# Optimization experiments

Measured on AMD Instinct MI355X. Metric: run time of the kernel, lower is better.

The kernel has to match this reference:

```python
import jax, jax.numpy as jnp
import numpy as np

N = 200000
B = 2
GX, GY, GZ = 480, 360, 32          # full-res voxel grid for input_coords
GX2, GY2, GZ2 = 240, 180, 16       # output_scale grid for bxyz_indx
CIN, CR, COUT = 64, 64, 64
CR2 = CR // 2
P_SCALE = (2, 4, 6, 8)


def setup_inputs() -> dict:
    key = jax.random.key(0)
    ks = jax.random.split(key, 24)
    s = 0.05
    input_data = jax.random.normal(ks[0], (N, CIN), dtype=jnp.float32)
    bcol = jax.random.randint(ks[1], (N, 1), 0, B, dtype=jnp.int32)
    xc = jax.random.randint(ks[2], (N, 1), 0, GX, dtype=jnp.int32)
    yc = jax.random.randint(ks[3], (N, 1), 0, GY, dtype=jnp.int32)
    zc = jax.random.randint(ks[4], (N, 1), 0, GZ, dtype=jnp.int32)
    input_coords = jnp.concatenate([bcol, xc, yc, zc], axis=1)
    input_coords_inv = jax.random.randint(ks[5], (N,), 0, N, dtype=jnp.int32)
    b2 = jax.random.randint(ks[6], (N, 1), 0, B, dtype=jnp.int32)
    x2 = jax.random.randint(ks[7], (N, 1), 0, GX2, dtype=jnp.int32)
    y2 = jax.random.randint(ks[8], (N, 1), 0, GY2, dtype=jnp.int32)
    z2 = jax.random.randint(ks[9], (N, 1), 0, GZ2, dtype=jnp.int32)
    bxyz_indx = jnp.concatenate([b2, x2, y2, z2], axis=1)
    # parameters (torch Linear stored here as [in, out])
    W_red = jax.random.normal(ks[10], (CIN, CR)) * s
    b_red = jnp.zeros((CR,), jnp.float32)
    fc_list_W = jax.random.normal(ks[11], (4, CR, CR2)) * s
    fc_list_b = jnp.zeros((4, CR2), jnp.float32)
    fcs_W = jax.random.normal(ks[12], (4, CR2, CR2)) * s
    fcs_b = jnp.zeros((4, CR2), jnp.float32)
    fc_W = jax.random.normal(ks[13], (CR2, CR2)) * s
    out_fc_W = jax.random.normal(ks[14], (CR2, CR)) * s
    lo_W1 = jax.random.normal(ks[15], (2 * CR, CR)) * s
    lo_W2 = jax.random.normal(ks[16], (CR, COUT)) * s
    lo_b2 = jnp.zeros((COUT,), jnp.float32)
    return dict(input_data=input_data, input_coords=input_coords,
                input_coords_inv=input_coords_inv, bxyz_indx=bxyz_indx,
                W_red=W_red, b_red=b_red, fc_list_W=fc_list_W, fc_list_b=fc_list_b,
                fcs_W=fcs_W, fcs_b=fcs_b, fc_W=fc_W, out_fc_W=out_fc_W,
                lo_W1=lo_W1, lo_W2=lo_W2, lo_b2=lo_b2)


def _segment_mean(x, seg, num_segments):
    sums = jax.ops.segment_sum(x, seg, num_segments=num_segments)
    cnt = jax.ops.segment_sum(jnp.ones((x.shape[0], 1), x.dtype), seg,
                              num_segments=num_segments)
    return sums / jnp.maximum(cnt, 1.0)


def reference(input_data, input_coords, input_coords_inv, bxyz_indx,
              W_red, b_red, fc_list_W, fc_list_b, fcs_W, fcs_b,
              fc_W, out_fc_W, lo_W1, lo_W2, lo_b2):
    reduced = jax.nn.relu(input_data @ W_red + b_red)          # [N, CR]
    bcol = input_coords[:, 0]
    xyz = input_coords[:, 1:]
    outs = []
    for j, ps in enumerate(P_SCALE):
        dx = (GX - 1) // ps + 1
        dy = (GY - 1) // ps + 1
        dz = (GZ - 1) // ps + 1
        q = xyz // ps                                          # [N, 3]
        # dense linearized voxel id replaces torch.unique(return_inverse)
        lin = ((bcol * dx + q[:, 0]) * dy + q[:, 1]) * dz + q[:, 2]
        nseg = B * dx * dy * dz
        fkm = _segment_mean(reduced, lin, nseg)                # [nseg, CR]
        att = jax.nn.relu(fkm @ fc_list_W[j] + fc_list_b[j])   # [nseg, CR2]
        outs.append(att[lin])                                  # gather back [N, CR2]
    scale_features = jnp.stack(outs, axis=1)                   # [N, 4, CR2]
    feat_S = scale_features.sum(axis=1)                        # [N, CR2]
    feat_Z = jax.nn.relu(feat_S @ fc_W)                        # [N, CR2]
    att_v = jax.nn.sigmoid(jnp.einsum('nc,kcd->nkd', feat_Z, fcs_W) + fcs_b)
    fused = (scale_features * att_v).sum(axis=1) @ out_fc_W    # [N, CR]
    output_f = jnp.concatenate([reduced, fused], axis=1)       # [N, 2*CR]
    proj = jax.nn.relu(output_f @ lo_W1) @ lo_W2 + lo_b2       # [N, COUT]
    proj = proj[input_coords_inv]
    # with_fm branch: index = (b, z, y, x) of bxyz_indx (b,x,y,z)
    lin2 = ((bxyz_indx[:, 0] * GZ2 + bxyz_indx[:, 3]) * GY2
            + bxyz_indx[:, 2]) * GX2 + bxyz_indx[:, 1]
    tv_fmap = jax.ops.segment_max(proj, lin2, num_segments=B * GZ2 * GY2 * GX2)
    tv_fmap = jnp.where(jnp.isneginf(tv_fmap), 0.0, tv_fmap)   # empty voxels -> 0
    return proj, tv_fmap, lin2
```

## Files before the change

### kernel.cpp

```cpp
#include <hip/hip_runtime.h>
#include <math.h>

#define NPTS   200000
#define CR     64
#define CR2    32

#define NSEG0      1382400
#define SUM123_ROW2 172800
#define SUM123_ROW3 230400
#define SUM123_ROWS 252000

#define TVSEG  1382400
#define GX2    240
#define GY2    180
#define GZ2    16

#define NBATCH 21600

__device__ __forceinline__ float bcastf(float v, int l) {
    return __int_as_float(__builtin_amdgcn_readlane(__float_as_int(v), l));
}

__device__ __forceinline__ int lin_scale(int b, int x, int y, int z,
                                         int ps, int dx, int dy, int dz) {
    int qx = x / ps, qy = y / ps, qz = z / ps;
    return ((b * dx + qx) * dy + qy) * dz + qz;
}

__device__ __forceinline__ void seg_decode(int seg, int& l1, int& l2, int& l3) {
    int qz = seg & 15; int rest = seg >> 4;
    int qy = rest % 180; int rest2 = rest / 180;
    int qx = rest2 % 240; int bb = rest2 / 240;
    l1 = ((bb * 120 + (qx >> 1)) * 90 + (qy >> 1)) * 8 + (qz >> 1);
    l2 = ((bb *  80 + (qx / 3)) * 60 + (qy / 3)) * 6 + (qz / 3);
    l3 = ((bb *  60 + (qx >> 2)) * 45 + (qy >> 2)) * 4 + (qz >> 2);
}

__global__ __launch_bounds__(256) void k_reduced(
        const float* __restrict__ in, const float* __restrict__ Wred,
        const float* __restrict__ bred, float* __restrict__ red) {
    __shared__ float Wl[CR * CR];
    for (int i = threadIdx.x; i < CR * CR; i += blockDim.x) Wl[i] = Wred[i];
    __syncthreads();
    int lane = threadIdx.x & 63;
    float bl = bred[lane];
    int wid  = blockIdx.x * 4 + (threadIdx.x >> 6);
    int nw   = gridDim.x * 4;
    for (int p = wid; p < NPTS / 2; p += nw) {
        int r0 = 2 * p, r1 = r0 + 1;
        float x0 = in[(size_t)r0 * CR + lane];
        float x1 = in[(size_t)r1 * CR + lane];
        float acc0 = bl, acc1 = bl;
#pragma unroll
        for (int k = 0; k < CR; ++k) {
            float w = Wl[k * CR + lane];
            acc0 += bcastf(x0, k) * w;
            acc1 += bcastf(x1, k) * w;
        }
        red[(size_t)r0 * CR + lane] = fmaxf(acc0, 0.f);
        red[(size_t)r1 * CR + lane] = fmaxf(acc1, 0.f);
    }
}

__global__ __launch_bounds__(256) void k_scatter(
        const float* __restrict__ red, const int* __restrict__ coords,
        float* __restrict__ sum0, float* __restrict__ cnt) {
    int lane = threadIdx.x & 63;
    int wid  = blockIdx.x * 4 + (threadIdx.x >> 6);
    int nw   = gridDim.x * 4;
    for (int r = wid; r < NPTS; r += nw) {
        int4 c = ((const int4*)coords)[r];
        int l0 = lin_scale(c.x, c.y, c.z, c.w, 2, 240, 180, 16);
        float v = red[(size_t)r * CR + lane];
        atomicAdd(&sum0[(size_t)l0 * CR + lane], v);
        if (lane == 0) atomicAdd(&cnt[l0], 1.0f);
    }
}

__global__ __launch_bounds__(256) void k_gatt(
        const float* __restrict__ sum0, float* __restrict__ attbuf,
        const float* __restrict__ cnt,
        const float* __restrict__ fcW, const float* __restrict__ fcB) {
    __shared__ float sw[3 * CR * CR2];
    for (int i = threadIdx.x; i < 3 * CR * CR2; i += blockDim.x)
        sw[i] = fcW[CR * CR2 + i];
    __syncthreads();
    int lane = threadIdx.x & 63;
    int d = lane & 31;
    int wid = blockIdx.x * 4 + (threadIdx.x >> 6);
    int nw  = gridDim.x * 4;
    for (int s = wid; s < SUM123_ROWS; s += nw) {
        int childLin = -1;
        const float* w; float bj;
        if (s < SUM123_ROW2) {
            int qz = s & 7, t = s >> 3;
            int qy = t % 90, t2 = t / 90;
            int qx = t2 % 120, b = t2 / 120;
            if (lane < 8) {
                int i = (lane >> 2) & 1, j = (lane >> 1) & 1, k = lane & 1;
                childLin = ((b * 240 + 2 * qx + i) * 180 + 2 * qy + j) * 16 + 2 * qz + k;
            }
            w = sw; bj = fcB[1 * CR2 + d];
        } else if (s < SUM123_ROW3) {
            int s2 = s - SUM123_ROW2;
            int qz = s2 % 6, t = s2 / 6;
            int qy = t % 60, t2 = t / 60;
            int qx = t2 % 80, b = t2 / 80;
            if (lane < 27) {
                int i = lane / 9, j = (lane / 3) % 3, k = lane % 3;
                int cz = 3 * qz + k;
                if (cz < 16)
                    childLin = ((b * 240 + 3 * qx + i) * 180 + 3 * qy + j) * 16 + cz;
            }
            w = sw + 2048; bj = fcB[2 * CR2 + d];
        } else {
            int s3 = s - SUM123_ROW3;
            int qz = s3 & 3, t = s3 >> 2;
            int qy = t % 45, t2 = t / 45;
            int qx = t2 % 60, b = t2 / 60;
            int i = lane >> 4, j = (lane >> 2) & 3, k = lane & 3;
            childLin = ((b * 240 + 4 * qx + i) * 180 + 4 * qy + j) * 16 + 4 * qz + k;
            w = sw + 4096; bj = fcB[3 * CR2 + d];
        }
        float myc = (childLin >= 0) ? cnt[childLin] : 0.f;
        unsigned long long mask = __ballot(myc > 0.f);
        if (!mask) continue;
        float ctot = myc;
        ctot += __shfl_xor(ctot, 1, 64);
        ctot += __shfl_xor(ctot, 2, 64);
        ctot += __shfl_xor(ctot, 4, 64);
        ctot += __shfl_xor(ctot, 8, 64);
        ctot += __shfl_xor(ctot, 16, 64);
        ctot += __shfl_xor(ctot, 32, 64);
        float acc = 0.f;
        while (mask) {
            int j = __ffsll((long long)mask) - 1; mask &= mask - 1;
            int cl = __builtin_amdgcn_readlane(childLin, j);
            acc += sum0[(size_t)cl * CR + lane];
        }
        float m = acc * (1.f / ctot);
        float p = bj;
#pragma unroll
        for (int k = 0; k < CR; ++k)
            p += bcastf(m, k) * w[k * CR2 + d];
        float att = fmaxf(p, 0.f);
        if (lane < 32) attbuf[(size_t)s * CR2 + lane] = att;
    }
}

__global__ __launch_bounds__(256) void k_att0(
        float* __restrict__ tv, const float* __restrict__ cnt,
        const float* __restrict__ fcW, const float* __restrict__ fcB) {
    __shared__ float sw[CR * CR2];
    for (int i = threadIdx.x; i < CR * CR2; i += blockDim.x) sw[i] = fcW[i];
    __syncthreads();
    int lane = threadIdx.x & 63;
    int d = lane & 31;
    int h = lane >> 5;
    float b0 = fcB[d];
    int wid = blockIdx.x * 4 + (threadIdx.x >> 6);
    int nw  = gridDim.x * 4;
    for (int batch = wid; batch < NBATCH; batch += nw) {
        int base = batch * 64;
        float c = cnt[base + lane];
        unsigned long long mask = __ballot(c > 0.f);
        while (mask) {
            int j0 = __ffsll((long long)mask) - 1; mask &= mask - 1;
            int j1 = j0, j2 = j0, j3 = j0;
            if (mask) { j1 = __ffsll((long long)mask) - 1; mask &= mask - 1;
              if (mask) { j2 = __ffsll((long long)mask) - 1; mask &= mask - 1;
                if (mask) { j3 = __ffsll((long long)mask) - 1; mask &= mask - 1; } } }
            float* row0 = tv + (size_t)(base + j0) * CR;
            float* row1 = tv + (size_t)(base + j1) * CR;
            float* row2 = tv + (size_t)(base + j2) * CR;
            float* row3 = tv + (size_t)(base + j3) * CR;
            float m0 = row0[lane] * (1.f / bcastf(c, j0));
            float m1 = row1[lane] * (1.f / bcastf(c, j1));
            float m2 = row2[lane] * (1.f / bcastf(c, j2));
            float m3 = row3[lane] * (1.f / bcastf(c, j3));
            float p0 = b0, p1 = b0, p2 = b0, p3 = b0;
#pragma unroll
            for (int k = 0; k < CR; ++k) {
                float wk = sw[k * CR2 + d];
                p0 += bcastf(m0, k) * wk;
                p1 += bcastf(m1, k) * wk;
                p2 += bcastf(m2, k) * wk;
                p3 += bcastf(m3, k) * wk;
            }
            float a0 = fmaxf(p0, 0.f), a1 = fmaxf(p1, 0.f);
            float a2 = fmaxf(p2, 0.f), a3 = fmaxf(p3, 0.f);
            float* rA = h ? row1 : row0; float vA = h ? a1 : a0;
            float* rB = h ? row3 : row2; float vB = h ? a3 : a2;
            rA[d] = vA;
            rB[d] = vB;
        }
    }
}

__global__ __launch_bounds__(1024) void k_mm(
        const float* __restrict__ outW, const float* __restrict__ loW1,
        float* __restrict__ M) {
    int e = threadIdx.x + blockIdx.x * 1024;
    if (e >= 2048) return;
    int r = e >> 6, c = e & 63;
    float acc = 0.f;
#pragma unroll
    for (int k = 0; k < 64; ++k)
        acc += outW[r * 64 + k] * loW1[(64 + k) * 64 + c];
    M[e] = acc;
}

__global__ __launch_bounds__(256) void k_seg(
        float* __restrict__ tv, const float* __restrict__ attbuf,
        const float* __restrict__ cnt,
        const float* __restrict__ fc_W, const float* __restrict__ fcsW,
        const float* __restrict__ fcsB, const float* __restrict__ M) {
    __shared__ float s_fcZ[1024];
    __shared__ float s_fcs[4096];
    __shared__ float s_M[2048];
    for (int i = threadIdx.x; i < 1024; i += 256) s_fcZ[i]  = fc_W[i];
    for (int i = threadIdx.x; i < 4096; i += 256) s_fcs[i]  = fcsW[i];
    for (int i = threadIdx.x; i < 2048; i += 256) s_M[i]    = M[i];
    __syncthreads();

    int lane = threadIdx.x & 63;
    int d = lane & 31;
    int h = lane >> 5;
    float vbA = fcsB[(h ? 1 : 0) * CR2 + d];
    float vbB = fcsB[(h ? 3 : 2) * CR2 + d];
    const float* VA = s_fcs + (h ? 1 : 0) * 1024;
    const float* VB = s_fcs + (h ? 3 : 2) * 1024;

    int wid = blockIdx.x * 4 + (threadIdx.x >> 6);
    int nw  = gridDim.x * 4;
    for (int batch = wid; batch < NBATCH; batch += nw) {
        int base = batch * 64;
        float c = cnt[base + lane];
        unsigned long long mask = __ballot(c > 0.f);
        while (mask) {
            int j0 = __ffsll((long long)mask) - 1; mask &= mask - 1;
            int n = 1, j1 = j0, j2 = j0, j3 = j0;
            if (mask) { j1 = __ffsll((long long)mask) - 1; mask &= mask - 1; n = 2;
              if (mask) { j2 = __ffsll((long long)mask) - 1; mask &= mask - 1; n = 3;
                if (mask) { j3 = __ffsll((long long)mask) - 1; mask &= mask - 1; n = 4; } } }
            int seg0 = base + j0, seg1 = base + j1, seg2 = base + j2, seg3 = base + j3;
            float* row0 = tv + (size_t)seg0 * CR;
            float* row1 = tv + (size_t)seg1 * CR;
            float* row2 = tv + (size_t)seg2 * CR;
            float* row3 = tv + (size_t)seg3 * CR;

            int l1_0, l2_0, l3_0, l1_1, l2_1, l3_1;
            int l1_2, l2_2, l3_2, l1_3, l2_3, l3_3;
            seg_decode(seg0, l1_0, l2_0, l3_0);
            seg_decode(seg1, l1_1, l2_1, l3_1);
            seg_decode(seg2, l1_2, l2_2, l3_2);
            seg_decode(seg3, l1_3, l2_3, l3_3);

            float a0_0 = row0[d];
            float a0_1 = row1[d];
            float a0_2 = row2[d];
            float a0_3 = row3[d];
            float a1_0 = attbuf[(size_t)l1_0 * CR2 + d];
            float a2_0 = attbuf[(size_t)(SUM123_ROW2 + l2_0) * CR2 + d];
            float a3_0 = attbuf[(size_t)(SUM123_ROW3 + l3_0) * CR2 + d];
            float a1_1 = attbuf[(size_t)l1_1 * CR2 + d];
            float a2_1 = attbuf[(size_t)(SUM123_ROW2 + l2_1) * CR2 + d];
            float a3_1 = attbuf[(size_t)(SUM123_ROW3 + l3_1) * CR2 + d];
            float a1_2 = attbuf[(size_t)l1_2 * CR2 + d];
            float a2_2 = attbuf[(size_t)(SUM123_ROW2 + l2_2) * CR2 + d];
            float a3_2 = attbuf[(size_t)(SUM123_ROW3 + l3_2) * CR2 + d];
            float a1_3 = attbuf[(size_t)l1_3 * CR2 + d];
            float a2_3 = attbuf[(size_t)(SUM123_ROW2 + l2_3) * CR2 + d];
            float a3_3 = attbuf[(size_t)(SUM123_ROW3 + l3_3) * CR2 + d];

            float fS0 = a0_0 + a1_0 + a2_0 + a3_0;
            float fS1 = a0_1 + a1_1 + a2_1 + a3_1;
            float fS2 = a0_2 + a1_2 + a2_2 + a3_2;
            float fS3 = a0_3 + a1_3 + a2_3 + a3_3;

            float z0 = 0.f, z1 = 0.f, z2 = 0.f, z3 = 0.f;
#pragma unroll
            for (int cc = 0; cc < CR2; ++cc) {
                float wz = s_fcZ[cc * CR2 + d];
                z0 += bcastf(fS0, cc) * wz;
                z1 += bcastf(fS1, cc) * wz;
                z2 += bcastf(fS2, cc) * wz;
                z3 += bcastf(fS3, cc) * wz;
            }
            float fZ0 = fmaxf(z0, 0.f), fZ1 = fmaxf(z1, 0.f);
            float fZ2 = fmaxf(z2, 0.f), fZ3 = fmaxf(z3, 0.f);

            float avA0 = vbA, avA1 = vbA, avA2 = vbA, avA3 = vbA;
            float avB0 = vbB, avB1 = vbB, avB2 = vbB, avB3 = vbB;
#pragma unroll
            for (int cc = 0; cc < CR2; ++cc) {
                float wa = VA[cc * CR2 + d];
                float wb = VB[cc * CR2 + d];
                float f0 = bcastf(fZ0, cc), f1 = bcastf(fZ1, cc);
                float f2 = bcastf(fZ2, cc), f3 = bcastf(fZ3, cc);
                avA0 += f0 * wa; avB0 += f0 * wb;
                avA1 += f1 * wa; avB1 += f1 * wb;
                avA2 += f2 * wa; avB2 += f2 * wb;
                avA3 += f3 * wa; avB3 += f3 * wb;
            }
            avA0 = 1.f / (1.f + __expf(-avA0)); avB0 = 1.f / (1.f + __expf(-avB0));
            avA1 = 1.f / (1.f + __expf(-avA1)); avB1 = 1.f / (1.f + __expf(-avB1));
            avA2 = 1.f / (1.f + __expf(-avA2)); avB2 = 1.f / (1.f + __expf(-avB2));
            avA3 = 1.f / (1.f + __expf(-avA3)); avB3 = 1.f / (1.f + __expf(-avB3));

            float u0 = (h ? a1_0 : a0_0) * avA0 + (h ? a3_0 : a2_0) * avB0;
            float u1 = (h ? a1_1 : a0_1) * avA1 + (h ? a3_1 : a2_1) * avB1;
            float u2 = (h ? a1_2 : a0_2) * avA2 + (h ? a3_2 : a2_2) * avB2;
            float u3 = (h ? a1_3 : a0_3) * avA3 + (h ? a3_3 : a2_3) * avB3;
            float fI0 = u0 + __shfl_xor(u0, 32, 64);
            float fI1 = u1 + __shfl_xor(u1, 32, 64);
            float fI2 = u2 + __shfl_xor(u2, 32, 64);
            float fI3 = u3 + __shfl_xor(u3, 32, 64);

            float g0 = 0.f, g1 = 0.f, g2 = 0.f, g3 = 0.f;
#pragma unroll
            for (int dd = 0; dd < CR2; ++dd) {
                float wm = s_M[dd * CR + lane];
                g0 += bcastf(fI0, dd) * wm;
                g1 += bcastf(fI1, dd) * wm;
                g2 += bcastf(fI2, dd) * wm;
                g3 += bcastf(fI3, dd) * wm;
            }
            row0[lane] = g0;
            if (n > 1) row1[lane] = g1;
            if (n > 2) row2[lane] = g2;
            if (n > 3) row3[lane] = g3;
        }
    }
}

__global__ __launch_bounds__(256) void k_pg(
        const float* __restrict__ red, const float* __restrict__ gtab,
        const int* __restrict__ coords, const int* __restrict__ inv,
        const float* __restrict__ loW1, const float* __restrict__ loW2,
        const float* __restrict__ lob2, float* __restrict__ outProj) {
    __shared__ float s_W1[4096];
    __shared__ float s_W2[4096];
    for (int i = threadIdx.x; i < 4096; i += 256) s_W1[i] = loW1[i];
    for (int i = threadIdx.x; i < 4096; i += 256) s_W2[i] = loW2[i];
    __syncthreads();

    int lane = threadIdx.x & 63;
    float lob = lob2[lane];
    int wid = blockIdx.x * 4 + (threadIdx.x >> 6);
    int nw  = gridDim.x * 4;
    for (int q = wid; q < NPTS / 4; q += nw) {
        int i0 = 4 * q, i1 = i0 + 1, i2 = i0 + 2, i3 = i0 + 3;
        int s0 = inv[i0], s1 = inv[i1], s2 = inv[i2], s3 = inv[i3];
        int4 c0 = ((const int4*)coords)[s0];
        int4 c1 = ((const int4*)coords)[s1];
        int4 c2 = ((const int4*)coords)[s2];
        int4 c3 = ((const int4*)coords)[s3];
        int l0 = lin_scale(c0.x, c0.y, c0.z, c0.w, 2, 240, 180, 16);
        int l1 = lin_scale(c1.x, c1.y, c1.z, c1.w, 2, 240, 180, 16);
        int l2 = lin_scale(c2.x, c2.y, c2.z, c2.w, 2, 240, 180, 16);
        int l3 = lin_scale(c3.x, c3.y, c3.z, c3.w, 2, 240, 180, 16);

        float x0 = red[(size_t)s0 * CR + lane];
        float x1 = red[(size_t)s1 * CR + lane];
        float x2 = red[(size_t)s2 * CR + lane];
        float x3 = red[(size_t)s3 * CR + lane];
        float h0 = gtab[(size_t)l0 * CR + lane];
        float h1 = gtab[(size_t)l1 * CR + lane];
        float h2 = gtab[(size_t)l2 * CR + lane];
        float h3 = gtab[(size_t)l3 * CR + lane];
#pragma unroll
        for (int k = 0; k < CR; ++k) {
            float w = s_W1[k * CR + lane];
            h0 += bcastf(x0, k) * w;
            h1 += bcastf(x1, k) * w;
            h2 += bcastf(x2, k) * w;
            h3 += bcastf(x3, k) * w;
        }
        h0 = fmaxf(h0, 0.f); h1 = fmaxf(h1, 0.f);
        h2 = fmaxf(h2, 0.f); h3 = fmaxf(h3, 0.f);

        float q0 = lob, q1 = lob, q2 = lob, q3 = lob;
#pragma unroll
        for (int k = 0; k < CR; ++k) {
            float w = s_W2[k * CR + lane];
            q0 += bcastf(h0, k) * w;
            q1 += bcastf(h1, k) * w;
            q2 += bcastf(h2, k) * w;
            q3 += bcastf(h3, k) * w;
        }
        outProj[(size_t)i0 * CR + lane] = q0;
        outProj[(size_t)i1 * CR + lane] = q1;
        outProj[(size_t)i2 * CR + lane] = q2;
        outProj[(size_t)i3 * CR + lane] = q3;
    }
}

__global__ __launch_bounds__(256) void k_clear(
        float* __restrict__ tv, const float* __restrict__ cnt) {
    int lane = threadIdx.x & 63;
    int wid = blockIdx.x * 4 + (threadIdx.x >> 6);
    int nw = gridDim.x * 4;
    for (int batch = wid; batch < NBATCH; batch += nw) {
        int base = batch * 64;
        float c = cnt[base + lane];
        unsigned long long mask = __ballot(c > 0.f);
        while (mask) {
            int j = __ffsll((long long)mask) - 1; mask &= mask - 1;
            tv[(size_t)(base + j) * CR + lane] = 0.f;
        }
    }
}

__device__ __forceinline__ unsigned int fkey(float f) {
    unsigned int b = __float_as_uint(f);
    return (b & 0x80000000u) ? ~b : (b | 0x80000000u);
}

__global__ __launch_bounds__(256) void k_scatmax(
        const float* __restrict__ outProj, const int* __restrict__ bxyz,
        float* __restrict__ outLin, unsigned int* __restrict__ tvKey,
        unsigned char* __restrict__ flags) {
    int lane = threadIdx.x & 63;
    int wid  = blockIdx.x * 4 + (threadIdx.x >> 6);
    int nw   = gridDim.x * 4;
    for (int i = wid; i < NPTS; i += nw) {
        float v = outProj[(size_t)i * CR + lane];
        int4 c = ((const int4*)bxyz)[i];
        int lin2 = ((c.x * GZ2 + c.w) * GY2 + c.z) * GX2 + c.y;
        if (lane == 0) {
            outLin[i] = (float)lin2;
            flags[lin2] = 1;
        }
        atomicMax(&tvKey[(size_t)lin2 * CR + lane], fkey(v));
    }
}

__global__ __launch_bounds__(256) void k_fix(
        unsigned int* __restrict__ tv, const unsigned char* __restrict__ flags) {
    int lane = threadIdx.x & 63;
    int wid = blockIdx.x * 4 + (threadIdx.x >> 6);
    int nw  = gridDim.x * 4;
    for (int batch = wid; batch < NBATCH; batch += nw) {
        int base = batch * 64;
        unsigned char f = flags[base + lane];
        unsigned long long mask = __ballot(f != 0);
        while (mask) {
            int j = __ffsll((long long)mask) - 1; mask &= mask - 1;
            size_t idx = (size_t)(base + j) * CR + lane;
            unsigned int k = tv[idx];
            float v = (k == 0u) ? 0.f
                    : __uint_as_float((k & 0x80000000u) ? (k & 0x7FFFFFFFu) : ~k);
            ((float*)tv)[idx] = v;
        }
    }
}

extern "C" void kernel_launch(void* const* d_in, const int* in_sizes, int n_in,
                              void* d_out, int out_size, void* d_ws, size_t ws_size,
                              hipStream_t stream) {
    (void)in_sizes; (void)n_in; (void)out_size; (void)ws_size;
    const float* in_data = (const float*)d_in[0];
    const int*   coords  = (const int*)d_in[1];
    const int*   inv     = (const int*)d_in[2];
    const int*   bxyz    = (const int*)d_in[3];
    const float* W_red   = (const float*)d_in[4];
    const float* b_red   = (const float*)d_in[5];
    const float* fcW     = (const float*)d_in[6];
    const float* fcB     = (const float*)d_in[7];
    const float* fcsW    = (const float*)d_in[8];
    const float* fcsB    = (const float*)d_in[9];
    const float* fc_W    = (const float*)d_in[10];
    const float* outW    = (const float*)d_in[11];
    const float* loW1    = (const float*)d_in[12];
    const float* loW2    = (const float*)d_in[13];
    const float* lob2    = (const float*)d_in[14];

    float* outProj = (float*)d_out;
    float* tv      = outProj + (size_t)NPTS * CR;
    float* outLin  = tv + (size_t)TVSEG * CR;

    float* ws_f   = (float*)d_ws;
    float* red    = ws_f;
    float* attbuf = red + (size_t)NPTS * CR;
    float* cnt    = attbuf + (size_t)SUM123_ROWS * CR2;
    float* Mmat   = cnt + (size_t)NSEG0;
    unsigned char* flags = (unsigned char*)(Mmat + 2048);

    hipMemsetAsync(tv, 0, (size_t)TVSEG * CR * sizeof(float), stream);
    hipMemsetAsync(cnt, 0, (size_t)NSEG0 * sizeof(float), stream);
    hipMemsetAsync(flags, 0, (size_t)TVSEG, stream);

    k_mm<<<2, 1024, 0, stream>>>(outW, loW1, Mmat);
    k_reduced<<<1024, 256, 0, stream>>>(in_data, W_red, b_red, red);
    k_scatter<<<4096, 256, 0, stream>>>(red, coords, tv, cnt);
    k_gatt<<<2048, 256, 0, stream>>>(tv, attbuf, cnt, fcW, fcB);
    k_att0<<<2048, 256, 0, stream>>>(tv, cnt, fcW, fcB);
    k_seg<<<2048, 256, 0, stream>>>(tv, attbuf, cnt, fc_W, fcsW, fcsB, Mmat);
    k_pg<<<1024, 256, 0, stream>>>(red, tv, coords, inv, loW1, loW2, lob2, outProj);
    k_clear<<<512, 256, 0, stream>>>(tv, cnt);
    k_scatmax<<<1024, 256, 0, stream>>>(outProj, bxyz, outLin, (unsigned int*)tv, flags);
    k_fix<<<512, 256, 0, stream>>>((unsigned int*)tv, flags);
}
```

Baseline: 1.192 ms.

## Build compact occupied-segment list and fuse reduce/scatter and projection/scatter-max kernels

Fuses the reduction GEMM with the scale-0 scatter, and during that scatter builds a compact list of occupied segments plus a rank table. The att0 and seg kernels then iterate over that list instead of ballot-scanning all 1.38M segments, and write into compact buffers. att0 also clears the tv rows, which removes the separate clear kernel. The projection and scatter-max kernels are merged, so outProj is no longer re-read. In exchange the scatter gains a global atomic counter, list order becomes nondeterministic, and the gather in the projection kernel goes through an extra rank indirection.

```diff
diff --git a/kernel.cpp b/kernel.cpp
--- a/kernel.cpp
+++ b/kernel.cpp
@@ -36,9 +36,12 @@
     l3 = ((bb *  60 + (qx >> 2)) * 45 + (qy >> 2)) * 4 + (qz >> 2);
 }
 
-__global__ __launch_bounds__(256) void k_reduced(
-        const float* __restrict__ in, const float* __restrict__ Wred,
-        const float* __restrict__ bred, float* __restrict__ red) {
+__global__ __launch_bounds__(256) void k_redscat(
+        const float* __restrict__ in, const int* __restrict__ coords,
+        const float* __restrict__ Wred, const float* __restrict__ bred,
+        float* __restrict__ red, float* __restrict__ sum0,
+        float* __restrict__ cnt, int* __restrict__ list0,
+        int* __restrict__ listCount, int* __restrict__ rankArr) {
     __shared__ float Wl[CR * CR];
     for (int i = threadIdx.x; i < CR * CR; i += blockDim.x) Wl[i] = Wred[i];
     __syncthreads();
@@ -57,23 +60,27 @@
             acc0 += bcastf(x0, k) * w;
             acc1 += bcastf(x1, k) * w;
         }
-        red[(size_t)r0 * CR + lane] = fmaxf(acc0, 0.f);
-        red[(size_t)r1 * CR + lane] = fmaxf(acc1, 0.f);
-    }
-}
-
-__global__ __launch_bounds__(256) void k_scatter(
-        const float* __restrict__ red, const int* __restrict__ coords,
-        float* __restrict__ sum0, float* __restrict__ cnt) {
-    int lane = threadIdx.x & 63;
-    int wid  = blockIdx.x * 4 + (threadIdx.x >> 6);
-    int nw   = gridDim.x * 4;
-    for (int r = wid; r < NPTS; r += nw) {
-        int4 c = ((const int4*)coords)[r];
-        int l0 = lin_scale(c.x, c.y, c.z, c.w, 2, 240, 180, 16);
-        float v = red[(size_t)r * CR + lane];
-        atomicAdd(&sum0[(size_t)l0 * CR + lane], v);
-        if (lane == 0) atomicAdd(&cnt[l0], 1.0f);
+        acc0 = fmaxf(acc0, 0.f); acc1 = fmaxf(acc1, 0.f);
+        red[(size_t)r0 * CR + lane] = acc0;
+        red[(size_t)r1 * CR + lane] = acc1;
+        int4 c0 = ((const int4*)coords)[r0];
+        int4 c1 = ((const int4*)coords)[r1];
+        int l0a = lin_scale(c0.x, c0.y, c0.z, c0.w, 2, 240, 180, 16);
+        int l0b = lin_scale(c1.x, c1.y, c1.z, c1.w, 2, 240, 180, 16);
+        atomicAdd(&sum0[(size_t)l0a * CR + lane], acc0);
+        atomicAdd(&sum0[(size_t)l0b * CR + lane], acc1);
+        if (lane == 0) {
+            float olda = atomicAdd(&cnt[l0a], 1.0f);
+            if (olda == 0.f) {
+                int idx = atomicAdd(listCount, 1);
+                list0[idx] = l0a; rankArr[l0a] = idx;
+            }
+            float oldb = atomicAdd(&cnt[l0b], 1.0f);
+            if (oldb == 0.f) {
+                int idx = atomicAdd(listCount, 1);
+                list0[idx] = l0b; rankArr[l0b] = idx;
+            }
+        }
     }
 }
 
@@ -148,9 +155,11 @@
     }
 }
 
-__global__ __launch_bounds__(256) void k_att0(
+__global__ __launch_bounds__(256) void k_att0z(
         float* __restrict__ tv, const float* __restrict__ cnt,
-        const float* __restrict__ fcW, const float* __restrict__ fcB) {
+        const int* __restrict__ list0, const int* __restrict__ listCount,
+        const float* __restrict__ fcW, const float* __restrict__ fcB,
+        float* __restrict__ att0c) {
     __shared__ float sw[CR * CR2];
     for (int i = threadIdx.x; i < CR * CR2; i += blockDim.x) sw[i] = fcW[i];
     __syncthreads();
@@ -158,42 +167,38 @@
     int d = lane & 31;
     int h = lane >> 5;
     float b0 = fcB[d];
+    int total = listCount[0];
+    int ngroups = (total + 3) >> 2;
     int wid = blockIdx.x * 4 + (threadIdx.x >> 6);
     int nw  = gridDim.x * 4;
-    for (int batch = wid; batch < NBATCH; batch += nw) {
-        int base = batch * 64;
-        float c = cnt[base + lane];
-        unsigned long long mask = __ballot(c > 0.f);
-        while (mask) {
-            int j0 = __ffsll((long long)mask) - 1; mask &= mask - 1;
-            int j1 = j0, j2 = j0, j3 = j0;
-            if (mask) { j1 = __ffsll((long long)mask) - 1; mask &= mask - 1;
-              if (mask) { j2 = __ffsll((long long)mask) - 1; mask &= mask - 1;
-                if (mask) { j3 = __ffsll((long long)mask) - 1; mask &= mask - 1; } } }
-            float* row0 = tv + (size_t)(base + j0) * CR;
-            float* row1 = tv + (size_t)(base + j1) * CR;
-            float* row2 = tv + (size_t)(base + j2) * CR;
-            float* row3 = tv + (size_t)(base + j3) * CR;
-            float m0 = row0[lane] * (1.f / bcastf(c, j0));
-            float m1 = row1[lane] * (1.f / bcastf(c, j1));
-            float m2 = row2[lane] * (1.f / bcastf(c, j2));
-            float m3 = row3[lane] * (1.f / bcastf(c, j3));
-            float p0 = b0, p1 = b0, p2 = b0, p3 = b0;
-#pragma unroll
-            for (int k = 0; k < CR; ++k) {
-                float wk = sw[k * CR2 + d];
-                p0 += bcastf(m0, k) * wk;
-                p1 += bcastf(m1, k) * wk;
-                p2 += bcastf(m2, k) * wk;
-                p3 += bcastf(m3, k) * wk;
-            }
-            float a0 = fmaxf(p0, 0.f), a1 = fmaxf(p1, 0.f);
-            float a2 = fmaxf(p2, 0.f), a3 = fmaxf(p3, 0.f);
-            float* rA = h ? row1 : row0; float vA = h ? a1 : a0;
-            float* rB = h ? row3 : row2; float vB = h ? a3 : a2;
-            rA[d] = vA;
-            rB[d] = vB;
-        }
+    for (int g = wid; g < ngroups; g += nw) {
+        int r0 = 4 * g;
+        int r1 = min(r0 + 1, total - 1);
+        int r2 = min(r0 + 2, total - 1);
+        int r3 = min(r0 + 3, total - 1);
+        int s0 = list0[r0], s1 = list0[r1], s2 = list0[r2], s3 = list0[r3];
+        float* row0 = tv + (size_t)s0 * CR;
+        float* row1 = tv + (size_t)s1 * CR;
+        float* row2 = tv + (size_t)s2 * CR;
+        float* row3 = tv + (size_t)s3 * CR;
+        float m0 = row0[lane] * (1.f / cnt[s0]);
+        float m1 = row1[lane] * (1.f / cnt[s1]);
+        float m2 = row2[lane] * (1.f / cnt[s2]);
+        float m3 = row3[lane] * (1.f / cnt[s3]);
+        float p0 = b0, p1 = b0, p2 = b0, p3 = b0;
+#pragma unroll
+        for (int k = 0; k < CR; ++k) {
+            float wk = sw[k * CR2 + d];
+            p0 += bcastf(m0, k) * wk;
+            p1 += bcastf(m1, k) * wk;
+            p2 += bcastf(m2, k) * wk;
+            p3 += bcastf(m3, k) * wk;
+        }
+        float a0 = fmaxf(p0, 0.f), a1 = fmaxf(p1, 0.f);
+        float a2 = fmaxf(p2, 0.f), a3 = fmaxf(p3, 0.f);
+        att0c[(size_t)(h ? r2 : r0) * CR2 + d] = h ? a2 : a0;
+        att0c[(size_t)(h ? r3 : r1) * CR2 + d] = h ? a3 : a1;
+        row0[lane] = 0.f; row1[lane] = 0.f; row2[lane] = 0.f; row3[lane] = 0.f;
     }
 }
 
@@ -211,10 +216,11 @@
 }
 
 __global__ __launch_bounds__(256) void k_seg(
-        float* __restrict__ tv, const float* __restrict__ attbuf,
-        const float* __restrict__ cnt,
+        const int* __restrict__ list0, const int* __restrict__ listCount,
+        const float* __restrict__ att0c, const float* __restrict__ attbuf,
         const float* __restrict__ fc_W, const float* __restrict__ fcsW,
-        const float* __restrict__ fcsB, const float* __restrict__ M) {
+        const float* __restrict__ fcsB, const float* __restrict__ M,
+        float* __restrict__ gc) {
     __shared__ float s_fcZ[1024];
     __shared__ float s_fcs[4096];
     __shared__ float s_M[2048];
@@ -231,114 +237,115 @@
     const float* VA = s_fcs + (h ? 1 : 0) * 1024;
     const float* VB = s_fcs + (h ? 3 : 2) * 1024;
 
+    int total = listCount[0];
+    int ngroups = (total + 3) >> 2;
     int wid = blockIdx.x * 4 + (threadIdx.x >> 6);
     int nw  = gridDim.x * 4;
-    for (int batch = wid; batch < NBATCH; batch += nw) {
-        int base = batch * 64;
-        float c = cnt[base + lane];
-        unsigned long long mask = __ballot(c > 0.f);
-        while (mask) {
-            int j0 = __ffsll((long long)mask) - 1; mask &= mask - 1;
-            int n = 1, j1 = j0, j2 = j0, j3 = j0;
-            if (mask) { j1 = __ffsll((long long)mask) - 1; mask &= mask - 1; n = 2;
-              if (mask) { j2 = __ffsll((long long)mask) - 1; mask &= mask - 1; n = 3;
-                if (mask) { j3 = __ffsll((long long)mask) - 1; mask &= mask - 1; n = 4; } } }
-            int seg0 = base + j0, seg1 = base + j1, seg2 = base + j2, seg3 = base + j3;
-            float* row0 = tv + (size_t)seg0 * CR;
-            float* row1 = tv + (size_t)seg1 * CR;
-            float* row2 = tv + (size_t)seg2 * CR;
-            float* row3 = tv + (size_t)seg3 * CR;
-
-            int l1_0, l2_0, l3_0, l1_1, l2_1, l3_1;
-            int l1_2, l2_2, l3_2, l1_3, l2_3, l3_3;
-            seg_decode(seg0, l1_0, l2_0, l3_0);
-            seg_decode(seg1, l1_1, l2_1, l3_1);
-            seg_decode(seg2, l1_2, l2_2, l3_2);
-            seg_decode(seg3, l1_3, l2_3, l3_3);
-
-            float a0_0 = row0[d];
-            float a0_1 = row1[d];
-            float a0_2 = row2[d];
-            float a0_3 = row3[d];
-            float a1_0 = attbuf[(size_t)l1_0 * CR2 + d];
-            float a2_0 = attbuf[(size_t)(SUM123_ROW2 + l2_0) * CR2 + d];
-            float a3_0 = attbuf[(size_t)(SUM123_ROW3 + l3_0) * CR2 + d];
-            float a1_1 = attbuf[(size_t)l1_1 * CR2 + d];
-            float a2_1 = attbuf[(size_t)(SUM123_ROW2 + l2_1) * CR2 + d];
-            float a3_1 = attbuf[(size_t)(SUM123_ROW3 + l3_1) * CR2 + d];
-            float a1_2 = attbuf[(size_t)l1_2 * CR2 + d];
-            float a2_2 = attbuf[(size_t)(SUM123_ROW2 + l2_2) * CR2 + d];
-            float a3_2 = attbuf[(size_t)(SUM123_ROW3 + l3_2) * CR2 + d];
-            float a1_3 = attbuf[(size_t)l1_3 * CR2 + d];
-            float a2_3 = attbuf[(size_t)(SUM123_ROW2 + l2_3) * CR2 + d];
-            float a3_3 = attbuf[(size_t)(SUM123_ROW3 + l3_3) * CR2 + d];
-
-            float fS0 = a0_0 + a1_0 + a2_0 + a3_0;
-            float fS1 = a0_1 + a1_1 + a2_1 + a3_1;
-            float fS2 = a0_2 + a1_2 + a2_2 + a3_2;
-            float fS3 = a0_3 + a1_3 + a2_3 + a3_3;
-
-            float z0 = 0.f, z1 = 0.f, z2 = 0.f, z3 = 0.f;
-#pragma unroll
-            for (int cc = 0; cc < CR2; ++cc) {
-                float wz = s_fcZ[cc * CR2 + d];
-                z0 += bcastf(fS0, cc) * wz;
-                z1 += bcastf(fS1, cc) * wz;
-                z2 += bcastf(fS2, cc) * wz;
-                z3 += bcastf(fS3, cc) * wz;
-            }
-            float fZ0 = fmaxf(z0, 0.f), fZ1 = fmaxf(z1, 0.f);
-            float fZ2 = fmaxf(z2, 0.f), fZ3 = fmaxf(z3, 0.f);
-
-            float avA0 = vbA, avA1 = vbA, avA2 = vbA, avA3 = vbA;
-            float avB0 = vbB, avB1 = vbB, avB2 = vbB, avB3 = vbB;
-#pragma unroll
-            for (int cc = 0; cc < CR2; ++cc) {
-                float wa = VA[cc * CR2 + d];
-                float wb = VB[cc * CR2 + d];
-                float f0 = bcastf(fZ0, cc), f1 = bcastf(fZ1, cc);
-                float f2 = bcastf(fZ2, cc), f3 = bcastf(fZ3, cc);
-                avA0 += f0 * wa; avB0 += f0 * wb;
-                avA1 += f1 * wa; avB1 += f1 * wb;
-                avA2 += f2 * wa; avB2 += f2 * wb;
-                avA3 += f3 * wa; avB3 += f3 * wb;
-            }
-            avA0 = 1.f / (1.f + __expf(-avA0)); avB0 = 1.f / (1.f + __expf(-avB0));
-            avA1 = 1.f / (1.f + __expf(-avA1)); avB1 = 1.f / (1.f + __expf(-avB1));
-            avA2 = 1.f / (1.f + __expf(-avA2)); avB2 = 1.f / (1.f + __expf(-avB2));
-            avA3 = 1.f / (1.f + __expf(-avA3)); avB3 = 1.f / (1.f + __expf(-avB3));
-
-            float u0 = (h ? a1_0 : a0_0) * avA0 + (h ? a3_0 : a2_0) * avB0;
-            float u1 = (h ? a1_1 : a0_1) * avA1 + (h ? a3_1 : a2_1) * avB1;
-            float u2 = (h ? a1_2 : a0_2) * avA2 + (h ? a3_2 : a2_2) * avB2;
-            float u3 = (h ? a1_3 : a0_3) * avA3 + (h ? a3_3 : a2_3) * avB3;
-            float fI0 = u0 + __shfl_xor(u0, 32, 64);
-            float fI1 = u1 + __shfl_xor(u1, 32, 64);
-            float fI2 = u2 + __shfl_xor(u2, 32, 64);
-            float fI3 = u3 + __shfl_xor(u3, 32, 64);
-
-            float g0 = 0.f, g1 = 0.f, g2 = 0.f, g3 = 0.f;
-#pragma unroll
-            for (int dd = 0; dd < CR2; ++dd) {
-                float wm = s_M[dd * CR + lane];
-                g0 += bcastf(fI0, dd) * wm;
-                g1 += bcastf(fI1, dd) * wm;
-                g2 += bcastf(fI2, dd) * wm;
-                g3 += bcastf(fI3, dd) * wm;
-            }
-            row0[lane] = g0;
-            if (n > 1) row1[lane] = g1;
-            if (n > 2) row2[lane] = g2;
-            if (n > 3) row3[lane] = g3;
-        }
-    }
-}
-
-__global__ __launch_bounds__(256) void k_pg(
-        const float* __restrict__ red, const float* __restrict__ gtab,
+    for (int g = wid; g < ngroups; g += nw) {
+        int r0 = 4 * g;
+        int r1 = min(r0 + 1, total - 1);
+        int r2 = min(r0 + 2, total - 1);
+        int r3 = min(r0 + 3, total - 1);
+        int seg0 = list0[r0], seg1 = list0[r1], seg2 = list0[r2], seg3 = list0[r3];
+
+        int l1_0, l2_0, l3_0, l1_1, l2_1, l3_1;
+        int l1_2, l2_2, l3_2, l1_3, l2_3, l3_3;
+        seg_decode(seg0, l1_0, l2_0, l3_0);
+        seg_decode(seg1, l1_1, l2_1, l3_1);
+        seg_decode(seg2, l1_2, l2_2, l3_2);
+        seg_decode(seg3, l1_3, l2_3, l3_3);
+
+        float a0_0 = att0c[(size_t)r0 * CR2 + d];
+        float a0_1 = att0c[(size_t)r1 * CR2 + d];
+        float a0_2 = att0c[(size_t)r2 * CR2 + d];
+        float a0_3 = att0c[(size_t)r3 * CR2 + d];
+        float a1_0 = attbuf[(size_t)l1_0 * CR2 + d];
+        float a2_0 = attbuf[(size_t)(SUM123_ROW2 + l2_0) * CR2 + d];
+        float a3_0 = attbuf[(size_t)(SUM123_ROW3 + l3_0) * CR2 + d];
+        float a1_1 = attbuf[(size_t)l1_1 * CR2 + d];
+        float a2_1 = attbuf[(size_t)(SUM123_ROW2 + l2_1) * CR2 + d];
+        float a3_1 = attbuf[(size_t)(SUM123_ROW3 + l3_1) * CR2 + d];
+        float a1_2 = attbuf[(size_t)l1_2 * CR2 + d];
+        float a2_2 = attbuf[(size_t)(SUM123_ROW2 + l2_2) * CR2 + d];
+        float a3_2 = attbuf[(size_t)(SUM123_ROW3 + l3_2) * CR2 + d];
+        float a1_3 = attbuf[(size_t)l1_3 * CR2 + d];
+        float a2_3 = attbuf[(size_t)(SUM123_ROW2 + l2_3) * CR2 + d];
+        float a3_3 = attbuf[(size_t)(SUM123_ROW3 + l3_3) * CR2 + d];
+
+        float fS0 = a0_0 + a1_0 + a2_0 + a3_0;
+        float fS1 = a0_1 + a1_1 + a2_1 + a3_1;
+        float fS2 = a0_2 + a1_2 + a2_2 + a3_2;
+        float fS3 = a0_3 + a1_3 + a2_3 + a3_3;
+
+        float z0 = 0.f, z1 = 0.f, z2 = 0.f, z3 = 0.f;
+#pragma unroll
+        for (int cc = 0; cc < CR2; ++cc) {
+            float wz = s_fcZ[cc * CR2 + d];
+            z0 += bcastf(fS0, cc) * wz;
+            z1 += bcastf(fS1, cc) * wz;
+            z2 += bcastf(fS2, cc) * wz;
+            z3 += bcastf(fS3, cc) * wz;
+        }
+        float fZ0 = fmaxf(z0, 0.f), fZ1 = fmaxf(z1, 0.f);
+        float fZ2 = fmaxf(z2, 0.f), fZ3 = fmaxf(z3, 0.f);
+
+        float avA0 = vbA, avA1 = vbA, avA2 = vbA, avA3 = vbA;
+        float avB0 = vbB, avB1 = vbB, avB2 = vbB, avB3 = vbB;
+#pragma unroll
+        for (int cc = 0; cc < CR2; ++cc) {
+            float wa = VA[cc * CR2 + d];
+            float wb = VB[cc * CR2 + d];
+            float f0 = bcastf(fZ0, cc), f1 = bcastf(fZ1, cc);
+            float f2 = bcastf(fZ2, cc), f3 = bcastf(fZ3, cc);
+            avA0 += f0 * wa; avB0 += f0 * wb;
+            avA1 += f1 * wa; avB1 += f1 * wb;
+            avA2 += f2 * wa; avB2 += f2 * wb;
+            avA3 += f3 * wa; avB3 += f3 * wb;
+        }
+        avA0 = 1.f / (1.f + __expf(-avA0)); avB0 = 1.f / (1.f + __expf(-avB0));
+        avA1 = 1.f / (1.f + __expf(-avA1)); avB1 = 1.f / (1.f + __expf(-avB1));
+        avA2 = 1.f / (1.f + __expf(-avA2)); avB2 = 1.f / (1.f + __expf(-avB2));
+        avA3 = 1.f / (1.f + __expf(-avA3)); avB3 = 1.f / (1.f + __expf(-avB3));
+
+        float u0 = (h ? a1_0 : a0_0) * avA0 + (h ? a3_0 : a2_0) * avB0;
+        float u1 = (h ? a1_1 : a0_1) * avA1 + (h ? a3_1 : a2_1) * avB1;
+        float u2 = (h ? a1_2 : a0_2) * avA2 + (h ? a3_2 : a2_2) * avB2;
+        float u3 = (h ? a1_3 : a0_3) * avA3 + (h ? a3_3 : a2_3) * avB3;
+        float fI0 = u0 + __shfl_xor(u0, 32, 64);
+        float fI1 = u1 + __shfl_xor(u1, 32, 64);
+        float fI2 = u2 + __shfl_xor(u2, 32, 64);
+        float fI3 = u3 + __shfl_xor(u3, 32, 64);
+
+        float g0 = 0.f, g1 = 0.f, g2 = 0.f, g3 = 0.f;
+#pragma unroll
+        for (int dd = 0; dd < CR2; ++dd) {
+            float wm = s_M[dd * CR + lane];
+            g0 += bcastf(fI0, dd) * wm;
+            g1 += bcastf(fI1, dd) * wm;
+            g2 += bcastf(fI2, dd) * wm;
+            g3 += bcastf(fI3, dd) * wm;
+        }
+        gc[(size_t)r0 * CR + lane] = g0;
+        gc[(size_t)r1 * CR + lane] = g1;
+        gc[(size_t)r2 * CR + lane] = g2;
+        gc[(size_t)r3 * CR + lane] = g3;
+    }
+}
+
+__device__ __forceinline__ unsigned int fkey(float f) {
+    unsigned int b = __float_as_uint(f);
+    return (b & 0x80000000u) ? ~b : (b | 0x80000000u);
+}
+
+__global__ __launch_bounds__(256) void k_pgmax(
+        const float* __restrict__ red, const float* __restrict__ gc,
+        const int* __restrict__ rankArr,
         const int* __restrict__ coords, const int* __restrict__ inv,
+        const int* __restrict__ bxyz,
         const float* __restrict__ loW1, const float* __restrict__ loW2,
-        const float* __restrict__ lob2, float* __restrict__ outProj) {
+        const float* __restrict__ lob2, float* __restrict__ outProj,
+        float* __restrict__ outLin, unsigned int* __restrict__ tvKey,
+        unsigned char* __restrict__ flags) {
     __shared__ float s_W1[4096];
     __shared__ float s_W2[4096];
     for (int i = threadIdx.x; i < 4096; i += 256) s_W1[i] = loW1[i];
@@ -360,15 +367,17 @@
         int l1 = lin_scale(c1.x, c1.y, c1.z, c1.w, 2, 240, 180, 16);
         int l2 = lin_scale(c2.x, c2.y, c2.z, c2.w, 2, 240, 180, 16);
         int l3 = lin_scale(c3.x, c3.y, c3.z, c3.w, 2, 240, 180, 16);
+        int rk0 = rankArr[l0], rk1 = rankArr[l1];
+        int rk2 = rankArr[l2], rk3 = rankArr[l3];
 
         float x0 = red[(size_t)s0 * CR + lane];
         float x1 = red[(size_t)s1 * CR + lane];
         float x2 = red[(size_t)s2 * CR + lane];
         float x3 = red[(size_t)s3 * CR + lane];
-        float h0 = gtab[(size_t)l0 * CR + lane];
-        float h1 = gtab[(size_t)l1 * CR + lane];
-        float h2 = gtab[(size_t)l2 * CR + lane];
-        float h3 = gtab[(size_t)l3 * CR + lane];
+        float h0 = gc[(size_t)rk0 * CR + lane];
+        float h1 = gc[(size_t)rk1 * CR + lane];
+        float h2 = gc[(size_t)rk2 * CR + lane];
+        float h3 = gc[(size_t)rk3 * CR + lane];
 #pragma unroll
         for (int k = 0; k < CR; ++k) {
             float w = s_W1[k * CR + lane];
@@ -393,46 +402,25 @@
         outProj[(size_t)i1 * CR + lane] = q1;
         outProj[(size_t)i2 * CR + lane] = q2;
         outProj[(size_t)i3 * CR + lane] = q3;
-    }
-}
-
-__global__ __launch_bounds__(256) void k_clear(
-        float* __restrict__ tv, const float* __restrict__ cnt) {
-    int lane = threadIdx.x & 63;
-    int wid = blockIdx.x * 4 + (threadIdx.x >> 6);
-    int nw = gridDim.x * 4;
-    for (int batch = wid; batch < NBATCH; batch += nw) {
-        int base = batch * 64;
-        float c = cnt[base + lane];
-        unsigned long long mask = __ballot(c > 0.f);
-        while (mask) {
-            int j = __ffsll((long long)mask) - 1; mask &= mask - 1;
-            tv[(size_t)(base + j) * CR + lane] = 0.f;
-        }
-    }
-}
-
-__device__ __forceinline__ unsigned int fkey(float f) {
-    unsigned int b = __float_as_uint(f);
-    return (b & 0x80000000u) ? ~b : (b | 0x80000000u);
-}
-
-__global__ __launch_bounds__(256) void k_scatmax(
-        const float* __restrict__ outProj, const int* __restrict__ bxyz,
-        float* __restrict__ outLin, unsigned int* __restrict__ tvKey,
-        unsigned char* __restrict__ flags) {
-    int lane = threadIdx.x & 63;
-    int wid  = blockIdx.x * 4 + (threadIdx.x >> 6);
-    int nw   = gridDim.x * 4;
-    for (int i = wid; i < NPTS; i += nw) {
-        float v = outProj[(size_t)i * CR + lane];
-        int4 c = ((const int4*)bxyz)[i];
-        int lin2 = ((c.x * GZ2 + c.w) * GY2 + c.z) * GX2 + c.y;
+
+        int4 b0 = ((const int4*)bxyz)[i0];
+        int4 b1 = ((const int4*)bxyz)[i1];
+        int4 b2 = ((const int4*)bxyz)[i2];
+        int4 b3 = ((const int4*)bxyz)[i3];
+        int n0 = ((b0.x * GZ2 + b0.w) * GY2 + b0.z) * GX2 + b0.y;
+        int n1 = ((b1.x * GZ2 + b1.w) * GY2 + b1.z) * GX2 + b1.y;
+        int n2 = ((b2.x * GZ2 + b2.w) * GY2 + b2.z) * GX2 + b2.y;
+        int n3 = ((b3.x * GZ2 + b3.w) * GY2 + b3.z) * GX2 + b3.y;
         if (lane == 0) {
-            outLin[i] = (float)lin2;
-            flags[lin2] = 1;
-        }
-        atomicMax(&tvKey[(size_t)lin2 * CR + lane], fkey(v));
+            outLin[i0] = (float)n0; flags[n0] = 1;
+            outLin[i1] = (float)n1; flags[n1] = 1;
+            outLin[i2] = (float)n2; flags[n2] = 1;
+            outLin[i3] = (float)n3; flags[n3] = 1;
+        }
+        atomicMax(&tvKey[(size_t)n0 * CR + lane], fkey(q0));
+        atomicMax(&tvKey[(size_t)n1 * CR + lane], fkey(q1));
+        atomicMax(&tvKey[(size_t)n2 * CR + lane], fkey(q2));
+        atomicMax(&tvKey[(size_t)n3 * CR + lane], fkey(q3));
     }
 }
 
@@ -484,21 +472,27 @@
     float* red    = ws_f;
     float* attbuf = red + (size_t)NPTS * CR;
     float* cnt    = attbuf + (size_t)SUM123_ROWS * CR2;
-    float* Mmat   = cnt + (size_t)NSEG0;
+    int*   listCount = (int*)(cnt + (size_t)NSEG0);
+    int*   rankArr   = listCount + 4;
+    int*   list0     = rankArr + (size_t)NSEG0;
+    float* att0c  = (float*)(list0 + (size_t)NPTS);
+    float* gc     = att0c + (size_t)NPTS * CR2;
+    float* Mmat   = gc + (size_t)NPTS * CR;
     unsigned char* flags = (unsigned char*)(Mmat + 2048);
 
     hipMemsetAsync(tv, 0, (size_t)TVSEG * CR * sizeof(float), stream);
-    hipMemsetAsync(cnt, 0, (size_t)NSEG0 * sizeof(float), stream);
+    hipMemsetAsync(cnt, 0, ((size_t)NSEG0 + 4) * sizeof(float), stream);
     hipMemsetAsync(flags, 0, (size_t)TVSEG, stream);
 
     k_mm<<<2, 1024, 0, stream>>>(outW, loW1, Mmat);
-    k_reduced<<<1024, 256, 0, stream>>>(in_data, W_red, b_red, red);
-    k_scatter<<<4096, 256, 0, stream>>>(red, coords, tv, cnt);
+    k_redscat<<<1024, 256, 0, stream>>>(in_data, coords, W_red, b_red,
+                                        red, tv, cnt, list0, listCount, rankArr);
     k_gatt<<<2048, 256, 0, stream>>>(tv, attbuf, cnt, fcW, fcB);
-    k_att0<<<2048, 256, 0, stream>>>(tv, cnt, fcW, fcB);
-    k_seg<<<2048, 256, 0, stream>>>(tv, attbuf, cnt, fc_W, fcsW, fcsB, Mmat);
-    k_pg<<<1024, 256, 0, stream>>>(red, tv, coords, inv, loW1, loW2, lob2, outProj);
-    k_clear<<<512, 256, 0, stream>>>(tv, cnt);
-    k_scatmax<<<1024, 256, 0, stream>>>(outProj, bxyz, outLin, (unsigned int*)tv, flags);
+    k_att0z<<<1024, 256, 0, stream>>>(tv, cnt, list0, listCount, fcW, fcB, att0c);
+    k_seg<<<1024, 256, 0, stream>>>(list0, listCount, att0c, attbuf,
+                                    fc_W, fcsW, fcsB, Mmat, gc);
+    k_pgmax<<<1024, 256, 0, stream>>>(red, gc, rankArr, coords, inv, bxyz,
+                                      loW1, loW2, lob2, outProj,
+                                      outLin, (unsigned int*)tv, flags);
     k_fix<<<512, 256, 0, stream>>>((unsigned int*)tv, flags);
 }
```

Result: slower. 3.116 ms (+161.5%).
